# Optimization experiments

Hardware: AMD Instinct MI355X
Metric: run time of the kernel (lower is better)

## Reference

```python
import jax, jax.numpy as jnp
import numpy as np

LOG2 = float(np.log(2.0))

def ssp(x):
    # shifted softplus: ln(0.5*exp(x) + 0.5) = softplus(x) - ln(2)
    return jax.nn.softplus(x) - LOG2

N, A, F, R, E = 50000, 128, 128, 20, 1600000

def setup_inputs() -> dict:
    key = jax.random.key(0)
    ks = jax.random.split(key, 14)
    s = lambda fan_in: 1.0 / np.sqrt(fan_in)
    return {
        "x": jax.random.normal(ks[0], (N, A), dtype=jnp.float32),
        "f_ij": jax.random.uniform(ks[1], (E, R), dtype=jnp.float32),
        "rcut_ij": jax.random.uniform(ks[2], (E,), dtype=jnp.float32),
        "idx_i": jnp.sort(jax.random.randint(ks[3], (E,), 0, N)),
        "idx_j": jax.random.randint(ks[4], (E,), 0, N),
        # in2f: Dense(A -> F), no bias
        "W_in2f": jax.random.uniform(ks[5], (A, F), minval=-s(A), maxval=s(A), dtype=jnp.float32),
        # filter_network: Dense(R->F, ssp) then Dense(F->F)
        "W_f1": jax.random.uniform(ks[6], (R, F), minval=-s(R), maxval=s(R), dtype=jnp.float32),
        "b_f1": jnp.zeros((F,), dtype=jnp.float32),
        "W_f2": jax.random.uniform(ks[7], (F, F), minval=-s(F), maxval=s(F), dtype=jnp.float32),
        "b_f2": jnp.zeros((F,), dtype=jnp.float32),
        # f2out: Dense(F->A, ssp) then Dense(A->A)
        "W_o1": jax.random.uniform(ks[8], (F, A), minval=-s(F), maxval=s(F), dtype=jnp.float32),
        "b_o1": jnp.zeros((A,), dtype=jnp.float32),
        "W_o2": jax.random.uniform(ks[9], (A, A), minval=-s(A), maxval=s(A), dtype=jnp.float32),
        "b_o2": jnp.zeros((A,), dtype=jnp.float32),
    }

def reference(x, f_ij, rcut_ij, idx_i, idx_j,
              W_in2f, W_f1, b_f1, W_f2, b_f2, W_o1, b_o1, W_o2, b_o2):
    n_atoms = x.shape[0]
    # in2f projection (no bias): [N, A] -> [N, F]
    h = x @ W_in2f
    # filter MLP on edge RBF features: [E, R] -> [E, F]
    Wij = ssp(f_ij @ W_f1 + b_f1) @ W_f2 + b_f2
    Wij = Wij * rcut_ij[:, None]
    # gather neighbor features, modulate by filter, scatter-add to centers
    x_ij = h[idx_j] * Wij                                   # [E, F]
    agg = jax.ops.segment_sum(x_ij, idx_i, num_segments=n_atoms)  # [N, F]
    # f2out MLP: [N, F] -> [N, A]
    out = ssp(agg @ W_o1 + b_o1) @ W_o2 + b_o2
    return out
```

## Files before the change

kernel.cpp:

```cpp
#include <hip/hip_runtime.h>
#include <math.h>

#define LN2F 0.6931471805599453f
#define LOG2EF 1.4426950408889634f

typedef _Float16 half_t;
typedef _Float16 half4_t __attribute__((ext_vector_type(4)));
typedef _Float16 half8_t __attribute__((ext_vector_type(8)));
typedef __fp16 fp16x2 __attribute__((ext_vector_type(2)));
typedef __fp16 fp16x4 __attribute__((ext_vector_type(4)));
typedef __fp16 fp16x8 __attribute__((ext_vector_type(8)));
typedef float f32x4 __attribute__((ext_vector_type(4)));

__device__ __forceinline__ float sspf(float z) {
    return fmaxf(z, 0.f) + __logf(1.f + __expf(-fabsf(z))) - LN2F;
}
__device__ __forceinline__ half4_t cvt4(float x, float y, float z, float w) {
    half4_t r; r[0]=(half_t)x; r[1]=(half_t)y; r[2]=(half_t)z; r[3]=(half_t)w; return r;
}
__device__ __forceinline__ half8_t pk8(float a, float b, float c, float d,
                                       float e, float f, float g, float h) {
    fp16x2 p0 = __builtin_amdgcn_cvt_pkrtz(a, b);
    fp16x2 p1 = __builtin_amdgcn_cvt_pkrtz(c, d);
    fp16x2 p2 = __builtin_amdgcn_cvt_pkrtz(e, f);
    fp16x2 p3 = __builtin_amdgcn_cvt_pkrtz(g, h);
    fp16x4 lo = __builtin_shufflevector(p0, p1, 0, 1, 2, 3);
    fp16x4 hi = __builtin_shufflevector(p2, p3, 0, 1, 2, 3);
    fp16x8 v  = __builtin_shufflevector(lo, hi, 0, 1, 2, 3, 4, 5, 6, 7);
    return __builtin_bit_cast(half8_t, v);
}

__device__ __forceinline__ void load_lds16(const void* g, void* l) {
    __builtin_amdgcn_global_load_lds(
        (const __attribute__((address_space(1))) unsigned int*)g,
        (__attribute__((address_space(3))) unsigned int*)l, 16, 0, 0);
}

__device__ __forceinline__ int lbound(const int* __restrict__ a, int n, int key) {
    int lo = 0, hi = n;
    while (lo < hi) { int m = (lo + hi) >> 1; if (a[m] < key) lo = m + 1; else hi = m; }
    return lo;
}

__global__ __launch_bounds__(256) void prep_weights(
    const float* __restrict__ W_in2f, const float* __restrict__ W_f1,
    const float* __restrict__ W_f2, const float* __restrict__ W_o1,
    const float* __restrict__ W_o2,
    const float* __restrict__ b_f1, const float* __restrict__ b_f2,
    half_t* __restrict__ Wt_in2f, half_t* __restrict__ Wt_f1,
    half_t* __restrict__ W2L, half_t* __restrict__ Wt_o1,
    half_t* __restrict__ Wt_o2, float* __restrict__ b1sc, float* __restrict__ b2a)
{
    int b = blockIdx.x;
    if (b < 64) {
        int i = b*256 + threadIdx.x;
        Wt_in2f[i] = (half_t)W_in2f[(i & 127)*128 + (i >> 7)];
    } else if (b < 80) {
        int i = (b-64)*256 + threadIdx.x;
        int n = i >> 5, k = i & 31;
        Wt_f1[i] = (k < 20) ? (half_t)W_f1[k*128 + n] : (half_t)0.f;
    } else if (b < 144) {
        int i = (b-80)*256 + threadIdx.x;
        int j = i & 7, ln = (i >> 3) & 15, g = (i >> 7) & 3;
        int nt = (i >> 9) & 7, t = i >> 12;
        int k = 32*t + ((j < 4) ? (g*4 + j) : (16 + g*4 + (j - 4)));
        W2L[i] = (half_t)(LN2F * W_f2[k*128 + nt*16 + ln]);
    } else if (b < 208) {
        int i = (b-144)*256 + threadIdx.x;
        Wt_o1[i] = (half_t)W_o1[(i & 127)*128 + (i >> 7)];
    } else if (b < 272) {
        int i = (b-208)*256 + threadIdx.x;
        Wt_o2[i] = (half_t)W_o2[(i & 127)*128 + (i >> 7)];
    } else {
        int c = threadIdx.x;
        if (c < 128) {
            float s = 0.f;
            for (int k = 0; k < 128; ++k) s += W_f2[k*128 + c];
            b2a[c]  = b_f2[c] - LN2F * s;
            b1sc[c] = b_f1[c] * LOG2EF;
        }
    }
}

__global__ __launch_bounds__(256) void seg_starts(
    const int* __restrict__ idx_i, int* __restrict__ atom_start, int E, int N)
{
    int e = blockIdx.x * 256 + threadIdx.x;
    if (e >= E) return;
    int a = idx_i[e];
    int prev = (e == 0) ? -1 : idx_i[e - 1];
    for (int k = prev + 1; k <= a; ++k) atom_start[k] = e;
    if (e == E - 1)
        for (int k = a + 1; k <= N; ++k) atom_start[k] = E;
}

__global__ __launch_bounds__(256) void mfma_gemm_h(
    const float* __restrict__ A, const half_t* __restrict__ Bt,
    half_t* __restrict__ Ch, int nrows)
{
    const int tid = threadIdx.x;
    const int w = tid >> 6, l = tid & 63, g = l >> 4, ln = l & 15;
    const int r0 = blockIdx.x * 64;

    f32x4 acc[4][2];
    #pragma unroll
    for (int rf = 0; rf < 4; ++rf)
        #pragma unroll
        for (int cf = 0; cf < 2; ++cf) acc[rf][cf] = (f32x4)0.f;

    #pragma unroll
    for (int kk = 0; kk < 8; ++kk) {
        const int kb = kk * 16 + g * 4;
        half4_t a[4];
        #pragma unroll
        for (int rf = 0; rf < 4; ++rf) {
            int r = r0 + rf * 16 + ln;
            int rr = r < nrows ? r : nrows - 1;
            float4 av = *(const float4*)(A + (size_t)rr * 128 + kb);
            a[rf] = cvt4(av.x, av.y, av.z, av.w);
        }
        #pragma unroll
        for (int cf = 0; cf < 2; ++cf) {
            int n = w * 32 + cf * 16 + ln;
            half4_t b = *(const half4_t*)(Bt + (size_t)n * 128 + kb);
            #pragma unroll
            for (int rf = 0; rf < 4; ++rf)
                acc[rf][cf] = __builtin_amdgcn_mfma_f32_16x16x16f16(a[rf], b, acc[rf][cf], 0, 0, 0);
        }
    }
    #pragma unroll
    for (int cf = 0; cf < 2; ++cf) {
        int n = w * 32 + cf * 16 + ln;
        #pragma unroll
        for (int rf = 0; rf < 4; ++rf)
            #pragma unroll
            for (int reg = 0; reg < 4; ++reg) {
                int r = r0 + rf * 16 + g * 4 + reg;
                if (r < nrows) Ch[(size_t)r * 128 + n] = (half_t)acc[rf][cf][reg];
            }
    }
}

__global__ __launch_bounds__(256) void mfma_gemm2(
    const float* __restrict__ A, const half_t* __restrict__ Bt1,
    const float* __restrict__ bias1, const half_t* __restrict__ Bt2,
    const float* __restrict__ bias2, float* __restrict__ out, int nrows)
{
    __shared__ half_t ts[64][136];
    const int tid = threadIdx.x;
    const int w = tid >> 6, l = tid & 63, g = l >> 4, ln = l & 15;
    const int r0 = blockIdx.x * 64;

    f32x4 acc[4][2];
    #pragma unroll
    for (int rf = 0; rf < 4; ++rf)
        #pragma unroll
        for (int cf = 0; cf < 2; ++cf) acc[rf][cf] = (f32x4)0.f;
    #pragma unroll
    for (int kk = 0; kk < 8; ++kk) {
        const int kb = kk * 16 + g * 4;
        half4_t a[4];
        #pragma unroll
        for (int rf = 0; rf < 4; ++rf) {
            int r = r0 + rf * 16 + ln;
            int rr = r < nrows ? r : nrows - 1;
            float4 av = *(const float4*)(A + (size_t)rr * 128 + kb);
            a[rf] = cvt4(av.x, av.y, av.z, av.w);
        }
        #pragma unroll
        for (int cf = 0; cf < 2; ++cf) {
            int n = w * 32 + cf * 16 + ln;
            half4_t b = *(const half4_t*)(Bt1 + (size_t)n * 128 + kb);
            #pragma unroll
            for (int rf = 0; rf < 4; ++rf)
                acc[rf][cf] = __builtin_amdgcn_mfma_f32_16x16x16f16(a[rf], b, acc[rf][cf], 0, 0, 0);
        }
    }
    #pragma unroll
    for (int cf = 0; cf < 2; ++cf) {
        int n = w * 32 + cf * 16 + ln;
        float bv = bias1[n];
        #pragma unroll
        for (int rf = 0; rf < 4; ++rf)
            #pragma unroll
            for (int reg = 0; reg < 4; ++reg)
                ts[rf*16 + g*4 + reg][n] = (half_t)sspf(acc[rf][cf][reg] + bv);
    }
    __syncthreads();

    f32x4 acc2[4][2];
    #pragma unroll
    for (int rf = 0; rf < 4; ++rf)
        #pragma unroll
        for (int cf = 0; cf < 2; ++cf) acc2[rf][cf] = (f32x4)0.f;
    #pragma unroll
    for (int kk = 0; kk < 8; ++kk) {
        const int kb = kk * 16 + g * 4;
        half4_t a[4];
        #pragma unroll
        for (int rf = 0; rf < 4; ++rf)
            a[rf] = *(const half4_t*)&ts[rf*16 + ln][kb];
        #pragma unroll
        for (int cf = 0; cf < 2; ++cf) {
            int n = w * 32 + cf * 16 + ln;
            half4_t b = *(const half4_t*)(Bt2 + (size_t)n * 128 + kb);
            #pragma unroll
            for (int rf = 0; rf < 4; ++rf)
                acc2[rf][cf] = __builtin_amdgcn_mfma_f32_16x16x16f16(a[rf], b, acc2[rf][cf], 0, 0, 0);
        }
    }
    #pragma unroll
    for (int cf = 0; cf < 2; ++cf) {
        int n = w * 32 + cf * 16 + ln;
        float bv = bias2[n];
        #pragma unroll
        for (int rf = 0; rf < 4; ++rf)
            #pragma unroll
            for (int reg = 0; reg < 4; ++reg) {
                int r = r0 + rf * 16 + g * 4 + reg;
                if (r < nrows) out[(size_t)r * 128 + n] = acc2[rf][cf][reg] + bv;
            }
    }
}

__global__ __launch_bounds__(256, 2) void edge_kernel(
    const float* __restrict__ f_ij, const float* __restrict__ rcut,
    const int* __restrict__ idx_j,
    const half_t* __restrict__ Wt_f1, const float* __restrict__ b1sc,
    const half_t* __restrict__ W2L, const float* __restrict__ b2a,
    const half_t* __restrict__ hh, float* __restrict__ agg,
    const int* __restrict__ atom_start, int E, int N, int W)
{
    __shared__ __align__(16) half_t W2s[16384];
    __shared__ __align__(16) half_t hsh[4][2][2048];
    __shared__ float b1s[128];

    const int tid = threadIdx.x;
    const int w = tid >> 6, l = tid & 63, g = l >> 4, ln = l & 15;
    const int lnh = ln >> 3, lnlo = ln & 7;

    for (int i = tid; i < 2048; i += 256)
        ((float4*)W2s)[i] = ((const float4*)W2L)[i];
    if (tid < 128) b1s[tid] = b1sc[tid];
    __syncthreads();

    const int kg = blockIdx.x * 4 + w;
    const int aLo = lbound(atom_start, N + 1, (int)((size_t)kg * E / W));
    const int aHi = (kg == W - 1) ? N
                  : lbound(atom_start, N + 1, (int)((size_t)(kg + 1) * E / W));
    if (aLo >= aHi) return;

    half8_t w1f[8];
    #pragma unroll
    for (int rf = 0; rf < 8; ++rf) {
        half4_t lo = *(const half4_t*)(Wt_f1 + (size_t)(rf*16 + ln)*32 + g*4);
        half4_t hi = *(const half4_t*)(Wt_f1 + (size_t)(rf*16 + ln)*32 + 16 + g*4);
        w1f[rf] = __builtin_shufflevector(lo, hi, 0, 1, 2, 3, 4, 5, 6, 7);
    }

    float b2v[8];
    #pragma unroll
    for (int q = 0; q < 8; ++q) b2v[q] = b2a[q*16 + ln];

    int acur = aLo;
    int ends0 = atom_start[acur + 1];
    int ends1 = atom_start[min(acur + 2, N)];
    int ends2 = atom_start[min(acur + 3, N)];
    int cs = atom_start[acur];
    int ce = min(cs + 16, ends0);
    bool fl0 = (ce == ends0);
    int csn = ce;
    int cen = min(csn + 16, fl0 ? ends1 : ends0);

    int jvN[4];
    {
        int jv0[4];
        #pragma unroll
        for (int it = 0; it < 4; ++it)
            jv0[it] = idx_j[min(cs + 4*it + g, E - 1)];
        asm volatile("" ::: "memory");
        #pragma unroll
        for (int it = 0; it < 4; ++it)
            load_lds16(hh + (size_t)jv0[it]*128 + ((ln ^ (2*it)) << 3),
                       &hsh[w][0][it*512]);
        asm volatile("" ::: "memory");
    }
    float4 fA, fB;
    {
        int e = min(cs + ln, E - 1);
        fA = *(const float4*)(f_ij + (size_t)e*20 + g*4);
        fB = *(const float4*)(f_ij + (size_t)e*20 + 16);
    }
    float rc[4];
    #pragma unroll
    for (int r2 = 0; r2 < 4; ++r2) rc[r2] = rcut[min(cs + 4*g + r2, E - 1)];
    #pragma unroll
    for (int it = 0; it < 4; ++it) jvN[it] = idx_j[min(csn + 4*it + g, E - 1)];
    asm volatile("" ::: "memory");

    float racc[8];
    #pragma unroll
    for (int q = 0; q < 8; ++q) racc[q] = 0.f;
    int p = 0;

    while (acur < aHi) {
        asm volatile("" ::: "memory");
        #pragma unroll
        for (int it = 0; it < 4; ++it)
            load_lds16(hh + (size_t)jvN[it]*128 + ((ln ^ (2*it)) << 3),
                       &hsh[w][p^1][it*512]);
        asm volatile("s_waitcnt vmcnt(4)" ::: "memory");
        __builtin_amdgcn_sched_barrier(0);

        half4_t blo = cvt4(fA.x, fA.y, fA.z, fA.w);
        half4_t bhi;
        if (g == 0) bhi = cvt4(fB.x, fB.y, fB.z, fB.w);
        else { half4_t zz = {}; bhi = zz; }
        half8_t bf = __builtin_shufflevector(blo, bhi, 0, 1, 2, 3, 4, 5, 6, 7);
        float rcm[4];
        #pragma unroll
        for (int r2 = 0; r2 < 4; ++r2)
            rcm[r2] = (cs + 4*g + r2 < ce) ? rc[r2] : 0.f;
        const bool flushF = (ce == ends0);
        const bool f1 = (cen == (flushF ? ends1 : ends0));
        const int cs2 = cen;
        const int endsel = flushF ? (f1 ? ends2 : ends1) : (f1 ? ends1 : ends0);
        const int ce2 = min(cs2 + 16, endsel);

        int jv2[4];
        #pragma unroll
        for (int it = 0; it < 4; ++it)
            jv2[it] = idx_j[min(cs2 + 4*it + g, E - 1)];
        float4 fA1, fB1;
        {
            int e = min(csn + ln, E - 1);
            fA1 = *(const float4*)(f_ij + (size_t)e*20 + g*4);
            fB1 = *(const float4*)(f_ij + (size_t)e*20 + 16);
        }
        float rc1[4];
        #pragma unroll
        for (int r2 = 0; r2 < 4; ++r2) rc1[r2] = rcut[min(csn + 4*g + r2, E - 1)];
        const int aeL = atom_start[min(acur + 4, N)];
        asm volatile("" ::: "memory");

        f32x4 z[8];
        #pragma unroll
        for (int rf = 0; rf < 8; ++rf)
            z[rf] = __builtin_amdgcn_mfma_f32_16x16x32_f16(w1f[rf], bf, (f32x4)0.f, 0, 0, 0);
        half8_t a2[4];
        #pragma unroll
        for (int t = 0; t < 4; ++t) {
            float4 bbA = *(const float4*)&b1s[(2*t)*16 + g*4];
            float4 bbB = *(const float4*)&b1s[(2*t+1)*16 + g*4];
            float l0 = __log2f(1.f + exp2f(fmaf(z[2*t][0],   LOG2EF, bbA.x)));
            float l1 = __log2f(1.f + exp2f(fmaf(z[2*t][1],   LOG2EF, bbA.y)));
            float l2 = __log2f(1.f + exp2f(fmaf(z[2*t][2],   LOG2EF, bbA.z)));
            float l3 = __log2f(1.f + exp2f(fmaf(z[2*t][3],   LOG2EF, bbA.w)));
            float l4 = __log2f(1.f + exp2f(fmaf(z[2*t+1][0], LOG2EF, bbB.x)));
            float l5 = __log2f(1.f + exp2f(fmaf(z[2*t+1][1], LOG2EF, bbB.y)));
            float l6 = __log2f(1.f + exp2f(fmaf(z[2*t+1][2], LOG2EF, bbB.z)));
            float l7 = __log2f(1.f + exp2f(fmaf(z[2*t+1][3], LOG2EF, bbB.w)));
            a2[t] = pk8(l0, l1, l2, l3, l4, l5, l6, l7);
        }

        f32x4 acc[4];
        #pragma unroll
        for (int q = 0; q < 4; ++q) { f32x4 t = {b2v[q], b2v[q], b2v[q], b2v[q]}; acc[q] = t; }
        __builtin_amdgcn_s_setprio(1);
        #pragma unroll
        for (int t = 0; t < 4; ++t)
            #pragma unroll
            for (int q = 0; q < 4; ++q) {
                half8_t bw = *(const half8_t*)&W2s[(((t*8 + q)*4 + g)*16 + ln)*8];
                acc[q] = __builtin_amdgcn_mfma_f32_16x16x32_f16(a2[t], bw, acc[q], 0, 0, 0);
            }
        __builtin_amdgcn_s_setprio(0);

        #pragma unroll
        for (int q = 0; q < 4; ++q) {
            float s = 0.f;
            #pragma unroll
            for (int r2 = 0; r2 < 4; ++r2) {
                int segp = (2*q + lnh) ^ (2*g);
                float hv = (float)hsh[w][p][(4*g + r2)*128 + segp*8 + lnlo];
                s = fmaf(acc[q][r2] * rcm[r2], hv, s);
            }
            racc[q] += s;
        }

        #pragma unroll
        for (int q = 0; q < 4; ++q) { f32x4 t = {b2v[4+q], b2v[4+q], b2v[4+q], b2v[4+q]}; acc[q] = t; }
        __builtin_amdgcn_s_setprio(1);
        #pragma unroll
        for (int t = 0; t < 4; ++t)
            #pragma unroll
            for (int q = 0; q < 4; ++q) {
                half8_t bw = *(const half8_t*)&W2s[(((t*8 + 4 + q)*4 + g)*16 + ln)*8];
                acc[q] = __builtin_amdgcn_mfma_f32_16x16x32_f16(a2[t], bw, acc[q], 0, 0, 0);
            }
        __builtin_amdgcn_s_setprio(0);
        #pragma unroll
        for (int q = 0; q < 4; ++q) {
            int nt = 4 + q;
            float s = 0.f;
            #pragma unroll
            for (int r2 = 0; r2 < 4; ++r2) {
                int segp = (2*nt + lnh) ^ (2*g);
                float hv = (float)hsh[w][p][(4*g + r2)*128 + segp*8 + lnlo];
                s = fmaf(acc[q][r2] * rcm[r2], hv, s);
            }
            racc[nt] += s;
        }

        if (flushF) {
            #pragma unroll
            for (int q = 0; q < 8; ++q) {
                float r = racc[q];
                r += __shfl_xor(r, 16, 64);
                r += __shfl_xor(r, 32, 64);
                racc[q] = r;
            }
            if (g == 0) {
                #pragma unroll
                for (int q = 0; q < 8; ++q)
                    agg[(size_t)acur*128 + q*16 + ln] = racc[q];
            }
            #pragma unroll
            for (int q = 0; q < 8; ++q) racc[q] = 0.f;
            ++acur;
            ends0 = ends1; ends1 = ends2; ends2 = aeL;
        }

        cs = csn; ce = cen; csn = cs2; cen = ce2;
        #pragma unroll
        for (int it = 0; it < 4; ++it) jvN[it] = jv2[it];
        fA = fA1; fB = fB1;
        #pragma unroll
        for (int r2 = 0; r2 < 4; ++r2) rc[r2] = rc1[r2];
        p ^= 1;
    }
}

extern "C" void kernel_launch(void* const* d_in, const int* in_sizes, int n_in,
                              void* d_out, int out_size, void* d_ws, size_t ws_size,
                              hipStream_t stream)
{
    const float* x      = (const float*)d_in[0];
    const float* f_ij   = (const float*)d_in[1];
    const float* rcut   = (const float*)d_in[2];
    const int*   idx_i  = (const int*)d_in[3];
    const int*   idx_j  = (const int*)d_in[4];
    const float* W_in2f = (const float*)d_in[5];
    const float* W_f1   = (const float*)d_in[6];
    const float* b_f1   = (const float*)d_in[7];
    const float* W_f2   = (const float*)d_in[8];
    const float* b_f2   = (const float*)d_in[9];
    const float* W_o1   = (const float*)d_in[10];
    const float* b_o1   = (const float*)d_in[11];
    const float* W_o2   = (const float*)d_in[12];
    const float* b_o2   = (const float*)d_in[13];

    const int N = in_sizes[0] / 128;
    const int E = in_sizes[2];

    half_t* h16  = (half_t*)d_ws;
    half_t* wt   = (half_t*)((char*)d_ws + (size_t)N * 128 * 4);
    half_t* Wt_in2f = wt;
    half_t* Wt_f1   = wt + 16384;
    half_t* W2L     = wt + 16384 + 4096;
    half_t* Wt_o1   = W2L + 16384;
    half_t* Wt_o2   = Wt_o1 + 16384;
    float*  b1sc    = (float*)(Wt_o2 + 16384);
    float*  b2a     = b1sc + 128;
    int* atom_start = (int*)(b2a + 128);

    prep_weights<<<273, 256, 0, stream>>>(W_in2f, W_f1, W_f2, W_o1, W_o2,
                                          b_f1, b_f2,
                                          Wt_in2f, Wt_f1, W2L, Wt_o1, Wt_o2,
                                          b1sc, b2a);
    seg_starts<<<(E + 255) / 256, 256, 0, stream>>>(idx_i, atom_start, E, N);

    const int gn  = (N + 63) / 64;
    const int nbl = 512;
    const int W   = nbl * 4;

    mfma_gemm_h<<<gn, 256, 0, stream>>>(x, Wt_in2f, h16, N);

    edge_kernel<<<nbl, 256, 0, stream>>>(f_ij, rcut, idx_j,
                                         Wt_f1, b1sc, W2L, b2a,
                                         h16, (float*)d_out, atom_start, E, N, W);

    mfma_gemm2<<<gn, 256, 0, stream>>>((const float*)d_out, Wt_o1, b_o1,
                                       Wt_o2, b_o2, (float*)d_out, N);
}
```

Before: 267.4 us.

## Permute filter output columns so each lane owns 8 contiguous features

Reorders the W_f2 column layout so MFMA output tile q for lane ln maps to feature ln*8+q. Each lane can then read its neighbor features with one 16-byte LDS load per row, instead of eight scalar half loads, and write agg with two float4 stores. The two 4-tile MFMA passes merge into one 8-accumulator pass, and the LDS swizzle for the h gather changes to match. This cuts LDS instruction count and store count, at the cost of more live accumulator registers, which may pressure occupancy at launch_bounds(256,2).

```diff
diff --git a/kernel.cpp b/kernel.cpp
--- a/kernel.cpp
+++ b/kernel.cpp
@@ -64,7 +64,7 @@
         int j = i & 7, ln = (i >> 3) & 15, g = (i >> 7) & 3;
         int nt = (i >> 9) & 7, t = i >> 12;
         int k = 32*t + ((j < 4) ? (g*4 + j) : (16 + g*4 + (j - 4)));
-        W2L[i] = (half_t)(LN2F * W_f2[k*128 + nt*16 + ln]);
+        W2L[i] = (half_t)(LN2F * W_f2[k*128 + ln*8 + nt]);
     } else if (b < 208) {
         int i = (b-144)*256 + threadIdx.x;
         Wt_o1[i] = (half_t)W_o1[(i & 127)*128 + (i >> 7)];
@@ -237,7 +237,6 @@
 
     const int tid = threadIdx.x;
     const int w = tid >> 6, l = tid & 63, g = l >> 4, ln = l & 15;
-    const int lnh = ln >> 3, lnlo = ln & 7;
 
     for (int i = tid; i < 2048; i += 256)
         ((float4*)W2s)[i] = ((const float4*)W2L)[i];
@@ -258,9 +257,17 @@
         w1f[rf] = __builtin_shufflevector(lo, hi, 0, 1, 2, 3, 4, 5, 6, 7);
     }
 
-    float b2v[8];
-    #pragma unroll
-    for (int q = 0; q < 8; ++q) b2v[q] = b2a[q*16 + ln];
+    f32x4 b2acc[8];
+    {
+        float4 blo4 = *(const float4*)(b2a + ln*8);
+        float4 bhi4 = *(const float4*)(b2a + ln*8 + 4);
+        float bv[8] = {blo4.x, blo4.y, blo4.z, blo4.w, bhi4.x, bhi4.y, bhi4.z, bhi4.w};
+        #pragma unroll
+        for (int q = 0; q < 8; ++q) {
+            f32x4 t = {bv[q], bv[q], bv[q], bv[q]};
+            b2acc[q] = t;
+        }
+    }
 
     int acur = aLo;
     int ends0 = atom_start[acur + 1];
@@ -281,7 +288,7 @@
         asm volatile("" ::: "memory");
         #pragma unroll
         for (int it = 0; it < 4; ++it)
-            load_lds16(hh + (size_t)jv0[it]*128 + ((ln ^ (2*it)) << 3),
+            load_lds16(hh + (size_t)jv0[it]*128 + ((ln ^ it) << 3),
                        &hsh[w][0][it*512]);
         asm volatile("" ::: "memory");
     }
@@ -307,7 +314,7 @@
         asm volatile("" ::: "memory");
         #pragma unroll
         for (int it = 0; it < 4; ++it)
-            load_lds16(hh + (size_t)jvN[it]*128 + ((ln ^ (2*it)) << 3),
+            load_lds16(hh + (size_t)jvN[it]*128 + ((ln ^ it) << 3),
                        &hsh[w][p^1][it*512]);
         asm volatile("s_waitcnt vmcnt(4)" ::: "memory");
         __builtin_amdgcn_sched_barrier(0);
@@ -363,53 +370,26 @@
             a2[t] = pk8(l0, l1, l2, l3, l4, l5, l6, l7);
         }
 
-        f32x4 acc[4];
-        #pragma unroll
-        for (int q = 0; q < 4; ++q) { f32x4 t = {b2v[q], b2v[q], b2v[q], b2v[q]}; acc[q] = t; }
+        f32x4 acc[8];
+        #pragma unroll
+        for (int q = 0; q < 8; ++q) acc[q] = b2acc[q];
         __builtin_amdgcn_s_setprio(1);
         #pragma unroll
         for (int t = 0; t < 4; ++t)
             #pragma unroll
-            for (int q = 0; q < 4; ++q) {
+            for (int q = 0; q < 8; ++q) {
                 half8_t bw = *(const half8_t*)&W2s[(((t*8 + q)*4 + g)*16 + ln)*8];
                 acc[q] = __builtin_amdgcn_mfma_f32_16x16x32_f16(a2[t], bw, acc[q], 0, 0, 0);
             }
         __builtin_amdgcn_s_setprio(0);
 
         #pragma unroll
-        for (int q = 0; q < 4; ++q) {
-            float s = 0.f;
-            #pragma unroll
-            for (int r2 = 0; r2 < 4; ++r2) {
-                int segp = (2*q + lnh) ^ (2*g);
-                float hv = (float)hsh[w][p][(4*g + r2)*128 + segp*8 + lnlo];
-                s = fmaf(acc[q][r2] * rcm[r2], hv, s);
-            }
-            racc[q] += s;
-        }
-
-        #pragma unroll
-        for (int q = 0; q < 4; ++q) { f32x4 t = {b2v[4+q], b2v[4+q], b2v[4+q], b2v[4+q]}; acc[q] = t; }
-        __builtin_amdgcn_s_setprio(1);
-        #pragma unroll
-        for (int t = 0; t < 4; ++t)
-            #pragma unroll
-            for (int q = 0; q < 4; ++q) {
-                half8_t bw = *(const half8_t*)&W2s[(((t*8 + 4 + q)*4 + g)*16 + ln)*8];
-                acc[q] = __builtin_amdgcn_mfma_f32_16x16x32_f16(a2[t], bw, acc[q], 0, 0, 0);
-            }
-        __builtin_amdgcn_s_setprio(0);
-        #pragma unroll
-        for (int q = 0; q < 4; ++q) {
-            int nt = 4 + q;
-            float s = 0.f;
-            #pragma unroll
-            for (int r2 = 0; r2 < 4; ++r2) {
-                int segp = (2*nt + lnh) ^ (2*g);
-                float hv = (float)hsh[w][p][(4*g + r2)*128 + segp*8 + lnlo];
-                s = fmaf(acc[q][r2] * rcm[r2], hv, s);
-            }
-            racc[nt] += s;
+        for (int r2 = 0; r2 < 4; ++r2) {
+            half8_t hv8 = *(const half8_t*)&hsh[w][p][(4*g + r2)*128 + ((ln ^ g) << 3)];
+            float rr = rcm[r2];
+            #pragma unroll
+            for (int q = 0; q < 8; ++q)
+                racc[q] = fmaf(acc[q][r2] * rr, (float)hv8[q], racc[q]);
         }
 
         if (flushF) {
@@ -421,9 +401,10 @@
                 racc[q] = r;
             }
             if (g == 0) {
-                #pragma unroll
-                for (int q = 0; q < 8; ++q)
-                    agg[(size_t)acur*128 + q*16 + ln] = racc[q];
+                float4 v0 = {racc[0], racc[1], racc[2], racc[3]};
+                float4 v1 = {racc[4], racc[5], racc[6], racc[7]};
+                *(float4*)(agg + (size_t)acur*128 + ln*8)     = v0;
+                *(float4*)(agg + (size_t)acur*128 + ln*8 + 4) = v1;
             }
             #pragma unroll
             for (int q = 0; q < 8; ++q) racc[q] = 0.f;
```

New measurement: 261.0 us. 2.4% less time.
